# Kernel tuning notes

Hardware: AMD Instinct MI355X
Metric: run time of the kernel (lower is better)

## Reference

```python
import jax, jax.numpy as jnp
import numpy as np


def _get_mask(in_features, out_features, in_flow_features, mask_type=None):
    # Faithful port of the torch get_mask() used by MADE.
    if mask_type == 'input':
        in_degrees = np.arange(in_features) % in_flow_features
    else:
        in_degrees = np.arange(in_features) % (in_flow_features - 1)
    if mask_type == 'output':
        out_degrees = np.arange(out_features) % in_flow_features - 1
    else:
        out_degrees = np.arange(out_features) % (in_flow_features - 1)
    return jnp.asarray((out_degrees[:, None] >= in_degrees[None, :]).astype(np.float32))


def setup_inputs() -> dict:
    B, D, H = 8192, 128, 2048
    key = jax.random.key(0)
    ks = jax.random.split(key, 7)
    w_scale_in = 1.0 / np.sqrt(D)
    w_scale_h = 1.0 / np.sqrt(H)
    return {
        'inputs': jax.random.normal(ks[0], (B, D), dtype=jnp.float32),
        's_w0': jax.random.normal(ks[1], (H, D), dtype=jnp.float32) * w_scale_in,
        's_b0': jnp.zeros((H,), dtype=jnp.float32),
        's_w1': jax.random.normal(ks[2], (H, H), dtype=jnp.float32) * w_scale_h,
        's_b1': jnp.zeros((H,), dtype=jnp.float32),
        's_w2': jax.random.normal(ks[3], (D, H), dtype=jnp.float32) * w_scale_h,
        's_b2': jnp.zeros((D,), dtype=jnp.float32),
        't_w0': jax.random.normal(ks[4], (H, D), dtype=jnp.float32) * w_scale_in,
        't_b0': jnp.zeros((H,), dtype=jnp.float32),
        't_w1': jax.random.normal(ks[5], (H, H), dtype=jnp.float32) * w_scale_h,
        't_b1': jnp.zeros((H,), dtype=jnp.float32),
        't_w2': jax.random.normal(ks[6], (D, H), dtype=jnp.float32) * w_scale_h,
        't_b2': jnp.zeros((D,), dtype=jnp.float32),
    }


def reference(inputs, s_w0, s_b0, s_w1, s_b1, s_w2, s_b2,
              t_w0, t_b0, t_w1, t_b1, t_w2, t_b2):
    # MADESplit forward, mode='direct', num_cond_inputs=None, pre_exp_tanh=False.
    D = inputs.shape[1]
    H = s_w0.shape[0]
    m_in = _get_mask(D, H, D, 'input')    # [H, D]
    m_h = _get_mask(H, H, D)              # [H, H]
    m_out = _get_mask(H, D, D, 'output')  # [D, H]

    def masked_mlp(w0, b0, w1, b1, w2, b2, act):
        h = act(inputs @ (m_in * w0).T + b0)   # joiner + first trunk activation
        h = act(h @ (m_h * w1).T + b1)
        return h @ (m_out * w2).T + b2

    m = masked_mlp(s_w0, s_b0, s_w1, s_b1, s_w2, s_b2, jnp.tanh)
    a = masked_mlp(t_w0, t_b0, t_w1, t_b1, t_w2, t_b2, jax.nn.relu)
    u = (inputs - m) * jnp.exp(-a)
    return u, -a.sum(-1, keepdims=True)
```

## Files before the change

### kernel.cpp

```cpp
#include <hip/hip_runtime.h>
#include <hip/hip_bf16.h>

typedef unsigned short u16;
typedef __attribute__((ext_vector_type(8))) short bf16x8;
typedef __attribute__((ext_vector_type(4))) float f32x4;

__device__ __forceinline__ u16 f2bf(float x) {
  union { float f; unsigned u; } v; v.f = x;
  unsigned r = v.u + 0x7fffu + ((v.u >> 16) & 1u);
  return (u16)(r >> 16);
}
__device__ __forceinline__ float bf2f(u16 h) {
  union { unsigned u; float f; } v; v.u = ((unsigned)h) << 16; return v.f;
}

__device__ __forceinline__ void gll16(const u16* g, u16* l) {
  __builtin_amdgcn_global_load_lds(
      (const __attribute__((address_space(1))) unsigned*)g,
      (__attribute__((address_space(3))) unsigned*)l, 16, 0, 0);
}

__device__ __forceinline__ f32x4 mfma_bb(bf16x8 a, bf16x8 b, f32x4 c) {
  return __builtin_amdgcn_mfma_f32_16x16x32_bf16(a, b, c, 0, 0, 0);
}

__global__ void prep_x(const float* __restrict__ x, u16* __restrict__ hi,
                       u16* __restrict__ lo, int n) {
  int i = blockIdx.x * 256 + threadIdx.x;
  if (i >= n) return;
  float v = x[i];
  u16 h = f2bf(v);
  hi[i] = h;
  lo[i] = f2bf(v - bf2f(h));
}

template <int MODE>
__global__ void prep_w(const float* __restrict__ w, u16* __restrict__ hi,
                       u16* __restrict__ lo, int rows, int cols) {
  int i = blockIdx.x * 256 + threadIdx.x;
  if (i >= rows * cols) return;
  int r = i / cols, c = i - r * cols;
  bool keep;
  if (MODE == 0)      keep = (r % 127) >= c;
  else if (MODE == 1) keep = (r % 127) >= (c % 127);
  else                keep = (r - 1) >= (c % 127);
  float v = keep ? w[i] : 0.0f;
  u16 h = f2bf(v);
  hi[i] = h;
  lo[i] = f2bf(v - bf2f(h));
}

template <int ACT>
__global__ __launch_bounds__(256, 2) void gemm_split(
    const u16* __restrict__ Ahi, const u16* __restrict__ Alo,
    const u16* __restrict__ Bhi, const u16* __restrict__ Blo,
    const float* __restrict__ bias,
    u16* __restrict__ Chi, u16* __restrict__ Clo,
    float* __restrict__ Cf,
    int M, int N, int K, int ksteps) {
  const int tid = threadIdx.x;
  const int l = tid & 63;
  const int w = tid >> 6;
  const int wr = w >> 1, wc = w & 1;
  const int bm = blockIdx.y * 128;
  const int bn = blockIdx.x * 128;
  const long kbase = (long)blockIdx.z * ksteps * 32;

  __shared__ __align__(16) u16 sAhi[4096];
  __shared__ __align__(16) u16 sAlo[4096];
  __shared__ __align__(16) u16 sBhi[4096];
  __shared__ __align__(16) u16 sBlo[4096];

  f32x4 acc[4][4] = {};

  const int srow = tid >> 2;
  const int scol = (tid & 3) << 3;
  const long aOff0 = (long)(bm + srow) * K + scol + kbase;
  const long aOff1 = aOff0 + 64L * K;
  const long bOff0 = (long)(bn + srow) * K + scol + kbase;
  const long bOff1 = bOff0 + 64L * K;
  const int ldst0 = tid * 8;
  const int ldst1 = 2048 + tid * 8;

  const int fr = l & 15, fq = l >> 4;

  for (int ks = 0; ks < ksteps; ++ks) {
    const long kk = (long)ks * 32;
    __syncthreads();
    gll16(Ahi + aOff0 + kk, sAhi + ldst0);
    gll16(Ahi + aOff1 + kk, sAhi + ldst1);
    gll16(Alo + aOff0 + kk, sAlo + ldst0);
    gll16(Alo + aOff1 + kk, sAlo + ldst1);
    gll16(Bhi + bOff0 + kk, sBhi + ldst0);
    gll16(Bhi + bOff1 + kk, sBhi + ldst1);
    gll16(Blo + bOff0 + kk, sBlo + ldst0);
    gll16(Blo + bOff1 + kk, sBlo + ldst1);
    __syncthreads();

    bf16x8 ah[4], alo[4], bh[4], blo[4];
#pragma unroll
    for (int m = 0; m < 4; ++m) {
      const int off = (wr * 64 + m * 16 + fr) * 32 + fq * 8;
      ah[m]  = *(const bf16x8*)(sAhi + off);
      alo[m] = *(const bf16x8*)(sAlo + off);
    }
#pragma unroll
    for (int n = 0; n < 4; ++n) {
      const int off = (wc * 64 + n * 16 + fr) * 32 + fq * 8;
      bh[n]  = *(const bf16x8*)(sBhi + off);
      blo[n] = *(const bf16x8*)(sBlo + off);
    }
#pragma unroll
    for (int m = 0; m < 4; ++m)
#pragma unroll
      for (int n = 0; n < 4; ++n) {
        acc[m][n] = mfma_bb(ah[m],  bh[n],  acc[m][n]);
        acc[m][n] = mfma_bb(alo[m], bh[n],  acc[m][n]);
        acc[m][n] = mfma_bb(ah[m],  blo[n], acc[m][n]);
      }
  }

  if (ACT == 2) {
    float* out = Cf + (long)blockIdx.z * M * N;
#pragma unroll
    for (int m = 0; m < 4; ++m) {
      const int row = bm + wr * 64 + m * 16 + fq * 4;
#pragma unroll
      for (int n = 0; n < 4; ++n) {
        const int col = bn + wc * 64 + n * 16 + fr;
#pragma unroll
        for (int r = 0; r < 4; ++r)
          out[(long)(row + r) * N + col] = acc[m][n][r];
      }
    }
  } else {
#pragma unroll
    for (int m = 0; m < 4; ++m) {
      const int row = bm + wr * 64 + m * 16 + fq * 4;
#pragma unroll
      for (int n = 0; n < 4; ++n) {
        const int col = bn + wc * 64 + n * 16 + fr;
        const float bv = bias[col];
#pragma unroll
        for (int r = 0; r < 4; ++r) {
          float z = acc[m][n][r] + bv;
          float h = (ACT == 0) ? tanhf(z) : fmaxf(z, 0.0f);
          u16 hi = f2bf(h);
          float rest = h - bf2f(hi);
          long idx = (long)(row + r) * N + col;
          Chi[idx] = hi;
          Clo[idx] = f2bf(rest);
        }
      }
    }
  }
}

__global__ void finalize_kernel(const float* __restrict__ x,
                                const float* __restrict__ pm,
                                const float* __restrict__ pa,
                                const float* __restrict__ sb2,
                                const float* __restrict__ tb2,
                                float* __restrict__ out_u,
                                float* __restrict__ out_s) {
  const int b = blockIdx.x * 4 + (threadIdx.x >> 6);
  const int l = threadIdx.x & 63;
  const long base = (long)b * 128;
  float m0 = sb2[l], m1 = sb2[64 + l];
  float a0 = tb2[l], a1 = tb2[64 + l];
#pragma unroll
  for (int k = 0; k < 4; ++k) {
    const long o = (long)k * (8192L * 128) + base;
    m0 += pm[o + l];      m1 += pm[o + 64 + l];
    a0 += pa[o + l];      a1 += pa[o + 64 + l];
  }
  out_u[base + l]      = (x[base + l]      - m0) * expf(-a0);
  out_u[base + 64 + l] = (x[base + 64 + l] - m1) * expf(-a1);
  float s = a0 + a1;
#pragma unroll
  for (int off = 32; off; off >>= 1) s += __shfl_down(s, off);
  if (l == 0) out_s[b] = -s;
}

extern "C" void kernel_launch(void* const* d_in, const int* in_sizes, int n_in,
                              void* d_out, int out_size, void* d_ws, size_t ws_size,
                              hipStream_t stream) {
  (void)in_sizes; (void)n_in; (void)out_size; (void)ws_size;
  const int B = 8192, D = 128, H = 2048;
  const float* x   = (const float*)d_in[0];
  const float* sw0 = (const float*)d_in[1];
  const float* sb0 = (const float*)d_in[2];
  const float* sw1 = (const float*)d_in[3];
  const float* sb1 = (const float*)d_in[4];
  const float* sw2 = (const float*)d_in[5];
  const float* sb2 = (const float*)d_in[6];
  const float* tw0 = (const float*)d_in[7];
  const float* tb0 = (const float*)d_in[8];
  const float* tw1 = (const float*)d_in[9];
  const float* tb1 = (const float*)d_in[10];
  const float* tw2 = (const float*)d_in[11];
  const float* tb2 = (const float*)d_in[12];

  char* ws = (char*)d_ws;
  size_t off = 0;
  auto alloc = [&](size_t bytes) {
    void* p = ws + off;
    off += (bytes + 255) & ~(size_t)255;
    return p;
  };
  u16* xhi  = (u16*)alloc((size_t)B * D * 2);
  u16* xlo  = (u16*)alloc((size_t)B * D * 2);
  u16* w0hi = (u16*)alloc((size_t)H * D * 2);
  u16* w0lo = (u16*)alloc((size_t)H * D * 2);
  u16* w1hi = (u16*)alloc((size_t)H * H * 2);
  u16* w1lo = (u16*)alloc((size_t)H * H * 2);
  u16* w2hi = (u16*)alloc((size_t)D * H * 2);
  u16* w2lo = (u16*)alloc((size_t)D * H * 2);
  u16* h1hi = (u16*)alloc((size_t)B * H * 2);
  u16* h1lo = (u16*)alloc((size_t)B * H * 2);
  u16* h2hi = (u16*)alloc((size_t)B * H * 2);
  u16* h2lo = (u16*)alloc((size_t)B * H * 2);
  float* pm = (float*)alloc((size_t)4 * B * D * 4);
  float* pa = (float*)alloc((size_t)4 * B * D * 4);

  float* out_u = (float*)d_out;
  float* out_s = out_u + (long)B * D;

  prep_x<<<(B * D + 255) / 256, 256, 0, stream>>>(x, xhi, xlo, B * D);

  auto run_mlp = [&](const float* w0, const float* b0, const float* w1,
                     const float* b1, const float* w2, float* part, bool is_tanh) {
    prep_w<0><<<(H * D + 255) / 256, 256, 0, stream>>>(w0, w0hi, w0lo, H, D);
    prep_w<1><<<(H * H + 255) / 256, 256, 0, stream>>>(w1, w1hi, w1lo, H, H);
    prep_w<2><<<(D * H + 255) / 256, 256, 0, stream>>>(w2, w2hi, w2lo, D, H);
    dim3 g12(H / 128, B / 128, 1);
    if (is_tanh) {
      gemm_split<0><<<g12, 256, 0, stream>>>(xhi, xlo, w0hi, w0lo, b0,
                                             h1hi, h1lo, nullptr, B, H, D, D / 32);
      gemm_split<0><<<g12, 256, 0, stream>>>(h1hi, h1lo, w1hi, w1lo, b1,
                                             h2hi, h2lo, nullptr, B, H, H, H / 32);
    } else {
      gemm_split<1><<<g12, 256, 0, stream>>>(xhi, xlo, w0hi, w0lo, b0,
                                             h1hi, h1lo, nullptr, B, H, D, D / 32);
      gemm_split<1><<<g12, 256, 0, stream>>>(h1hi, h1lo, w1hi, w1lo, b1,
                                             h2hi, h2lo, nullptr, B, H, H, H / 32);
    }
    dim3 g3(1, B / 128, 4);
    gemm_split<2><<<g3, 256, 0, stream>>>(h2hi, h2lo, w2hi, w2lo, nullptr,
                                          nullptr, nullptr, part, B, D, H,
                                          (H / 4) / 32);
  };

  run_mlp(sw0, sb0, sw1, sb1, sw2, pm, true);
  run_mlp(tw0, tb0, tw1, tb1, tw2, pa, false);

  finalize_kernel<<<B / 4, 256, 0, stream>>>(x, pm, pa, sb2, tb2, out_u, out_s);
}
```

Measured before the change: 672.7 us.

## Permute hidden units by mask degree to skip zero K-blocks in masked GEMMs

Hidden units are reordered by MADE degree so the masked weight matrices become block-triangular. Each GEMM tile then computes only the K range that can hold nonzero weights, skipping the masked-out work in the first two layers. Tiles are launched in reverse order so the heaviest ones start first. The separate prep kernels are also merged into one launch per MLP. This relies on exact degree arithmetic for D=128, H=2048, and the row/column permutation and tile bounds must match the mask exactly.

```diff
diff --git a/kernel.cpp b/kernel.cpp
--- a/kernel.cpp
+++ b/kernel.cpp
@@ -4,6 +4,8 @@
 typedef unsigned short u16;
 typedef __attribute__((ext_vector_type(8))) short bf16x8;
 typedef __attribute__((ext_vector_type(4))) float f32x4;
+
+constexpr int NB = 8192, ND = 128, NH = 2048;
 
 __device__ __forceinline__ u16 f2bf(float x) {
   union { float f; unsigned u; } v; v.f = x;
@@ -13,6 +15,24 @@
 __device__ __forceinline__ float bf2f(u16 h) {
   union { unsigned u; float f; } v; v.u = ((unsigned)h) << 16; return v.f;
 }
+__device__ __forceinline__ void store_split(u16* hi, u16* lo, long i, float v) {
+  u16 h = f2bf(v);
+  hi[i] = h;
+  lo[i] = f2bf(v - bf2f(h));
+}
+
+__device__ __forceinline__ int deg_sorted(int j) {
+  return (j < 272) ? (j / 17) : ((j - 16) >> 4);
+}
+__device__ __forceinline__ int perm_h(int j) {
+  int g, r;
+  if (j < 272) { g = j / 17; r = j - g * 17; }
+  else         { g = (j - 16) >> 4; r = (j - 16) & 15; }
+  return g + 127 * r;
+}
+__device__ __forceinline__ int offset_of_deg(int g) {
+  return (g < 16) ? 17 * g : 16 * g + 16;
+}
 
 __device__ __forceinline__ void gll16(const u16* g, u16* l) {
   __builtin_amdgcn_global_load_lds(
@@ -24,46 +44,87 @@
   return __builtin_amdgcn_mfma_f32_16x16x32_bf16(a, b, c, 0, 0, 0);
 }
 
-__global__ void prep_x(const float* __restrict__ x, u16* __restrict__ hi,
-                       u16* __restrict__ lo, int n) {
-  int i = blockIdx.x * 256 + threadIdx.x;
-  if (i >= n) return;
-  float v = x[i];
-  u16 h = f2bf(v);
-  hi[i] = h;
-  lo[i] = f2bf(v - bf2f(h));
-}
-
-template <int MODE>
-__global__ void prep_w(const float* __restrict__ w, u16* __restrict__ hi,
-                       u16* __restrict__ lo, int rows, int cols) {
-  int i = blockIdx.x * 256 + threadIdx.x;
-  if (i >= rows * cols) return;
-  int r = i / cols, c = i - r * cols;
-  bool keep;
-  if (MODE == 0)      keep = (r % 127) >= c;
-  else if (MODE == 1) keep = (r % 127) >= (c % 127);
-  else                keep = (r - 1) >= (c % 127);
-  float v = keep ? w[i] : 0.0f;
-  u16 h = f2bf(v);
-  hi[i] = h;
-  lo[i] = f2bf(v - bf2f(h));
-}
-
-template <int ACT>
+template <int PHASE>
+__global__ void prep_all(const float* __restrict__ x,
+                         const float* __restrict__ w0, const float* __restrict__ b0,
+                         const float* __restrict__ w1, const float* __restrict__ b1,
+                         const float* __restrict__ w2,
+                         u16* __restrict__ xhi, u16* __restrict__ xlo,
+                         u16* __restrict__ w0hi, u16* __restrict__ w0lo,
+                         u16* __restrict__ w1hi, u16* __restrict__ w1lo,
+                         u16* __restrict__ w2hi, u16* __restrict__ w2lo,
+                         float* __restrict__ b0p, float* __restrict__ b1p) {
+  constexpr int XB  = (NB * ND) / 256;
+  constexpr int W0B = (NH * ND) / 256;
+  constexpr int W1B = (NH * NH) / 256;
+  constexpr int W2B = (ND * NH) / 256;
+  constexpr int BB  = NH / 256;
+  int bid = blockIdx.x;
+  const int tid = threadIdx.x;
+
+  if (PHASE == 0) {
+    if (bid < XB) {
+      long i = (long)bid * 256 + tid;
+      store_split(xhi, xlo, i, x[i]);
+      return;
+    }
+    bid -= XB;
+  }
+  if (bid < W0B) {
+    int i = bid * 256 + tid;
+    int r_out = i >> 7, c = i & 127;
+    float v = (deg_sorted(r_out) >= c) ? w0[perm_h(r_out) * ND + c] : 0.0f;
+    store_split(w0hi, w0lo, i, v);
+    return;
+  }
+  bid -= W0B;
+  if (bid < W1B) {
+    long i = (long)bid * 256 + tid;
+    int r_out = (int)(i >> 11), c_out = (int)(i & 2047);
+    float v = (deg_sorted(r_out) >= deg_sorted(c_out))
+                  ? w1[(long)perm_h(r_out) * NH + perm_h(c_out)] : 0.0f;
+    store_split(w1hi, w1lo, i, v);
+    return;
+  }
+  bid -= W1B;
+  if (bid < W2B) {
+    int i = bid * 256 + tid;
+    int r = i >> 11, c_out = i & 2047;
+    float v = ((r - 1) >= deg_sorted(c_out)) ? w2[(r << 11) + perm_h(c_out)] : 0.0f;
+    store_split(w2hi, w2lo, i, v);
+    return;
+  }
+  bid -= W2B;
+  if (bid < BB) { int j = bid * 256 + tid; b0p[j] = b0[perm_h(j)]; return; }
+  bid -= BB;
+  { int j = bid * 256 + tid; b1p[j] = b1[perm_h(j)]; }
+}
+
+template <int ACT, int BOUND>
 __global__ __launch_bounds__(256, 2) void gemm_split(
     const u16* __restrict__ Ahi, const u16* __restrict__ Alo,
     const u16* __restrict__ Bhi, const u16* __restrict__ Blo,
     const float* __restrict__ bias,
     u16* __restrict__ Chi, u16* __restrict__ Clo,
     float* __restrict__ Cf,
-    int M, int N, int K, int ksteps) {
+    int M, int N, int K, int ksteps_arg) {
   const int tid = threadIdx.x;
   const int l = tid & 63;
   const int w = tid >> 6;
   const int wr = w >> 1, wc = w & 1;
   const int bm = blockIdx.y * 128;
-  const int bn = blockIdx.x * 128;
+  const int ntile = gridDim.x - 1 - blockIdx.x;
+  const int bn = ntile * 128;
+  int ksteps;
+  if (BOUND == 1) {
+    int ghi = deg_sorted(bn + 127);
+    ksteps = (ghi + 1 + 31) >> 5;
+  } else if (BOUND == 2) {
+    int ghi = deg_sorted(bn + 127);
+    ksteps = (offset_of_deg(ghi + 1) + 31) >> 5;
+  } else {
+    ksteps = ksteps_arg;
+  }
   const long kbase = (long)blockIdx.z * ksteps * 32;
 
   __shared__ __align__(16) u16 sAhi[4096];
@@ -145,11 +206,8 @@
         for (int r = 0; r < 4; ++r) {
           float z = acc[m][n][r] + bv;
           float h = (ACT == 0) ? tanhf(z) : fmaxf(z, 0.0f);
-          u16 hi = f2bf(h);
-          float rest = h - bf2f(hi);
           long idx = (long)(row + r) * N + col;
-          Chi[idx] = hi;
-          Clo[idx] = f2bf(rest);
+          store_split(Chi, Clo, idx, h);
         }
       }
     }
@@ -170,7 +228,7 @@
   float a0 = tb2[l], a1 = tb2[64 + l];
 #pragma unroll
   for (int k = 0; k < 4; ++k) {
-    const long o = (long)k * (8192L * 128) + base;
+    const long o = (long)k * ((long)NB * ND) + base;
     m0 += pm[o + l];      m1 += pm[o + 64 + l];
     a0 += pa[o + l];      a1 += pa[o + 64 + l];
   }
@@ -186,7 +244,6 @@
                               void* d_out, int out_size, void* d_ws, size_t ws_size,
                               hipStream_t stream) {
   (void)in_sizes; (void)n_in; (void)out_size; (void)ws_size;
-  const int B = 8192, D = 128, H = 2048;
   const float* x   = (const float*)d_in[0];
   const float* sw0 = (const float*)d_in[1];
   const float* sb0 = (const float*)d_in[2];
@@ -208,51 +265,59 @@
     off += (bytes + 255) & ~(size_t)255;
     return p;
   };
-  u16* xhi  = (u16*)alloc((size_t)B * D * 2);
-  u16* xlo  = (u16*)alloc((size_t)B * D * 2);
-  u16* w0hi = (u16*)alloc((size_t)H * D * 2);
-  u16* w0lo = (u16*)alloc((size_t)H * D * 2);
-  u16* w1hi = (u16*)alloc((size_t)H * H * 2);
-  u16* w1lo = (u16*)alloc((size_t)H * H * 2);
-  u16* w2hi = (u16*)alloc((size_t)D * H * 2);
-  u16* w2lo = (u16*)alloc((size_t)D * H * 2);
-  u16* h1hi = (u16*)alloc((size_t)B * H * 2);
-  u16* h1lo = (u16*)alloc((size_t)B * H * 2);
-  u16* h2hi = (u16*)alloc((size_t)B * H * 2);
-  u16* h2lo = (u16*)alloc((size_t)B * H * 2);
-  float* pm = (float*)alloc((size_t)4 * B * D * 4);
-  float* pa = (float*)alloc((size_t)4 * B * D * 4);
+  u16* xhi  = (u16*)alloc((size_t)NB * ND * 2);
+  u16* xlo  = (u16*)alloc((size_t)NB * ND * 2);
+  u16* w0hi = (u16*)alloc((size_t)NH * ND * 2);
+  u16* w0lo = (u16*)alloc((size_t)NH * ND * 2);
+  u16* w1hi = (u16*)alloc((size_t)NH * NH * 2);
+  u16* w1lo = (u16*)alloc((size_t)NH * NH * 2);
+  u16* w2hi = (u16*)alloc((size_t)ND * NH * 2);
+  u16* w2lo = (u16*)alloc((size_t)ND * NH * 2);
+  u16* h1hi = (u16*)alloc((size_t)NB * NH * 2);
+  u16* h1lo = (u16*)alloc((size_t)NB * NH * 2);
+  u16* h2hi = (u16*)alloc((size_t)NB * NH * 2);
+  u16* h2lo = (u16*)alloc((size_t)NB * NH * 2);
+  float* pm  = (float*)alloc((size_t)4 * NB * ND * 4);
+  float* pa  = (float*)alloc((size_t)4 * NB * ND * 4);
+  float* b0p = (float*)alloc((size_t)NH * 4);
+  float* b1p = (float*)alloc((size_t)NH * 4);
 
   float* out_u = (float*)d_out;
-  float* out_s = out_u + (long)B * D;
-
-  prep_x<<<(B * D + 255) / 256, 256, 0, stream>>>(x, xhi, xlo, B * D);
-
-  auto run_mlp = [&](const float* w0, const float* b0, const float* w1,
+  float* out_s = out_u + (long)NB * ND;
+
+  constexpr int XB  = (NB * ND) / 256;
+  constexpr int WSEG = (NH * ND) / 256 + (NH * NH) / 256 + (ND * NH) / 256 + 2 * (NH / 256);
+
+  auto run_mlp = [&](int phase, const float* w0, const float* b0, const float* w1,
                      const float* b1, const float* w2, float* part, bool is_tanh) {
-    prep_w<0><<<(H * D + 255) / 256, 256, 0, stream>>>(w0, w0hi, w0lo, H, D);
-    prep_w<1><<<(H * H + 255) / 256, 256, 0, stream>>>(w1, w1hi, w1lo, H, H);
-    prep_w<2><<<(D * H + 255) / 256, 256, 0, stream>>>(w2, w2hi, w2lo, D, H);
-    dim3 g12(H / 128, B / 128, 1);
+    if (phase == 0)
+      prep_all<0><<<XB + WSEG, 256, 0, stream>>>(x, w0, b0, w1, b1, w2,
+                                                 xhi, xlo, w0hi, w0lo, w1hi, w1lo,
+                                                 w2hi, w2lo, b0p, b1p);
+    else
+      prep_all<1><<<WSEG, 256, 0, stream>>>(x, w0, b0, w1, b1, w2,
+                                            xhi, xlo, w0hi, w0lo, w1hi, w1lo,
+                                            w2hi, w2lo, b0p, b1p);
+    dim3 g12(NH / 128, NB / 128, 1);
     if (is_tanh) {
-      gemm_split<0><<<g12, 256, 0, stream>>>(xhi, xlo, w0hi, w0lo, b0,
-                                             h1hi, h1lo, nullptr, B, H, D, D / 32);
-      gemm_split<0><<<g12, 256, 0, stream>>>(h1hi, h1lo, w1hi, w1lo, b1,
-                                             h2hi, h2lo, nullptr, B, H, H, H / 32);
+      gemm_split<0, 1><<<g12, 256, 0, stream>>>(xhi, xlo, w0hi, w0lo, b0p,
+                                                h1hi, h1lo, nullptr, NB, NH, ND, 0);
+      gemm_split<0, 2><<<g12, 256, 0, stream>>>(h1hi, h1lo, w1hi, w1lo, b1p,
+                                                h2hi, h2lo, nullptr, NB, NH, NH, 0);
     } else {
-      gemm_split<1><<<g12, 256, 0, stream>>>(xhi, xlo, w0hi, w0lo, b0,
-                                             h1hi, h1lo, nullptr, B, H, D, D / 32);
-      gemm_split<1><<<g12, 256, 0, stream>>>(h1hi, h1lo, w1hi, w1lo, b1,
-                                             h2hi, h2lo, nullptr, B, H, H, H / 32);
-    }
-    dim3 g3(1, B / 128, 4);
-    gemm_split<2><<<g3, 256, 0, stream>>>(h2hi, h2lo, w2hi, w2lo, nullptr,
-                                          nullptr, nullptr, part, B, D, H,
-                                          (H / 4) / 32);
+      gemm_split<1, 1><<<g12, 256, 0, stream>>>(xhi, xlo, w0hi, w0lo, b0p,
+                                                h1hi, h1lo, nullptr, NB, NH, ND, 0);
+      gemm_split<1, 2><<<g12, 256, 0, stream>>>(h1hi, h1lo, w1hi, w1lo, b1p,
+                                                h2hi, h2lo, nullptr, NB, NH, NH, 0);
+    }
+    dim3 g3(1, NB / 128, 4);
+    gemm_split<2, 0><<<g3, 256, 0, stream>>>(h2hi, h2lo, w2hi, w2lo, nullptr,
+                                             nullptr, nullptr, part, NB, ND, NH,
+                                             (NH / 4) / 32);
   };
 
-  run_mlp(sw0, sb0, sw1, sb1, sw2, pm, true);
-  run_mlp(tw0, tb0, tw1, tb1, tw2, pa, false);
-
-  finalize_kernel<<<B / 4, 256, 0, stream>>>(x, pm, pa, sb2, tb2, out_u, out_s);
-}
+  run_mlp(0, sw0, sb0, sw1, sb1, sw2, pm, true);
+  run_mlp(1, tw0, tb0, tw1, tb1, tw2, pa, false);
+
+  finalize_kernel<<<NB / 4, 256, 0, stream>>>(x, pm, pa, sb2, tb2, out_u, out_s);
+}
```

After: 609.9 us. 1.1x faster.
